# Kernel optimization log

Hardware: AMD Instinct MI355X
Metric: run time of the kernel (lower is better)

Reference implementation:

```python
import jax, jax.numpy as jnp
import numpy as np

KE = 14.3996454784255
P = 6  # polynomial cutoff order
A_EXP = 0.3
A_PREFACTOR = 0.4543
C = jnp.array([0.1818, 0.5099, 0.2802, 0.02817], dtype=jnp.float32)
K = jnp.array([3.2, 0.9423, 0.4028, 0.2016], dtype=jnp.float32)

N_NODES = 100000
N_EDGES = 6400000
N_ELEM = 10
N_RADII = 119


def setup_inputs() -> dict:
    key = jax.random.key(0)
    k1, k2, k3, k4, k5 = jax.random.split(key, 5)
    # edge distances in a physically plausible range (avoid x ~ 0 -> 1/x blowup)
    x = jax.random.uniform(k1, (N_EDGES, 1), dtype=jnp.float32) * 4.0 + 0.05
    node_attrs = jax.random.uniform(k2, (N_NODES, N_ELEM), dtype=jnp.float32)
    edge_index = jax.random.randint(k3, (2, N_EDGES), 0, N_NODES, dtype=jnp.int64)
    atomic_numbers = jax.random.randint(k4, (N_ELEM,), 1, N_RADII, dtype=jnp.int64)
    # covalent radii table (stand-in for ase.data.covalent_radii), ~0.3..2.6 Angstrom
    covalent_radii = 0.3 + 2.3 * jax.random.uniform(k5, (N_RADII,), dtype=jnp.float32)
    return {
        "x": x,
        "node_attrs": node_attrs,
        "edge_index": edge_index,
        "atomic_numbers": atomic_numbers,
        "covalent_radii": covalent_radii,
    }


def _envelope(x, r_max, p):
    r = x / r_max
    env = (1.0
           - (p + 1.0) * (p + 2.0) / 2.0 * r ** p
           + p * (p + 2.0) * r ** (p + 1)
           - p * (p + 1.0) / 2.0 * r ** (p + 2))
    return env * (x < r_max)


def reference(x, node_attrs, edge_index, atomic_numbers, covalent_radii):
    sender = edge_index[0]    # [E]
    receiver = edge_index[1]  # [E]
    # per-node atomic number from one-hot-ish node_attrs
    node_Z = atomic_numbers[jnp.argmax(node_attrs, axis=1)][:, None]  # [N,1] int
    Z_u = node_Z[sender]   # [E,1] int
    Z_v = node_Z[receiver] # [E,1] int
    Zu_f = Z_u.astype(x.dtype)
    Zv_f = Z_v.astype(x.dtype)
    a = A_PREFACTOR * 0.529 / (Zu_f ** A_EXP + Zv_f ** A_EXP)  # [E,1]
    r_over_a = x / a
    phi = (C[0] * jnp.exp(-K[0] * r_over_a)
           + C[1] * jnp.exp(-K[1] * r_over_a)
           + C[2] * jnp.exp(-K[2] * r_over_a)
           + C[3] * jnp.exp(-K[3] * r_over_a))
    v_edges = KE * Zu_f * Zv_f / x * phi  # [E,1]
    r_max = covalent_radii[Z_u[:, 0]][:, None] + covalent_radii[Z_v[:, 0]][:, None]  # [E,1]
    env = _envelope(x, r_max, float(P))
    v_edges = 0.5 * v_edges * env
    V_ZBL = jax.ops.segment_sum(v_edges, receiver, num_segments=node_attrs.shape[0])  # [N,1]
    return V_ZBL[:, 0]
```

## Files before the change

kernel.cpp:

```cpp
#include <hip/hip_runtime.h>

#define KE_CONST 14.3996454784255f

#define P2_SHIFT 15
#define P2_CHUNK 32768
#define MAXC     4
#define MAXE     16
#define ELEM_CAP 131072
#define DN_THR   1024
#define DN_BLOCKS 256
#define SCAN_THR 1024
#define SCAN_B   256
#define CNT_B    256
#define EB       32

__device__ __forceinline__ void scan_alloc(const unsigned* __restrict__ g_,
        int& nb0, int& nb1, int& nb2, int& nb3,
        int& st1, int& st2, int& st3,
        long long& g0, long long& g1, long long& g2, long long& g3) {
    g0 = g_[0]; g1 = g_[1]; g2 = g_[2]; g3 = g_[3];
    long long tot = g0 + g1 + g2 + g3; if (tot < 1) tot = 1;
    nb0 = (int)((g0 * SCAN_B) / tot); if (nb0 < 1) nb0 = 1;
    nb1 = (int)((g1 * SCAN_B) / tot); if (nb1 < 1) nb1 = 1;
    nb2 = (int)((g2 * SCAN_B) / tot); if (nb2 < 1) nb2 = 1;
    nb3 = (int)((g3 * SCAN_B) / tot); if (nb3 < 1) nb3 = 1;
    int sum = nb0 + nb1 + nb2 + nb3;
    while (sum > SCAN_B) {
        if      (nb0 >= nb1 && nb0 >= nb2 && nb0 >= nb3) nb0--;
        else if (nb1 >= nb2 && nb1 >= nb3)               nb1--;
        else if (nb2 >= nb3)                             nb2--;
        else                                             nb3--;
        sum--;
    }
    while (sum < SCAN_B) {
        if      (nb0 >= nb1 && nb0 >= nb2 && nb0 >= nb3) nb0++;
        else if (nb1 >= nb2 && nb1 >= nb3)               nb1++;
        else if (nb2 >= nb3)                             nb2++;
        else                                             nb3++;
        sum++;
    }
    st1 = nb0; st2 = nb0 + nb1; st3 = nb0 + nb1 + nb2;
}

__device__ __forceinline__ unsigned enc_val16(float xv, const float4& p) {
    float t = xv * p.x;
    float phi = 0.1818f  * __expf(-3.2f    * t)
              + 0.5099f  * __expf(-0.9423f * t)
              + 0.2802f  * __expf(-0.4028f * t)
              + 0.02817f * __expf(-0.2016f * t);
    float rr = xv * p.w;
    float r2 = rr * rr;
    float r6 = r2 * r2 * r2;
    float env = 1.0f - 28.0f * r6 + 48.0f * r6 * rr - 21.0f * r6 * r2;
    float val = fmaxf(p.y * phi / xv * env, 0.0f);
    unsigned e = (__float_as_uint(val) + 0x8000u) >> 16;
    return (xv < p.z) ? e : 0u;
}

__device__ __forceinline__ void scatter_bal(unsigned rw, float xv, const float4& p,
                                            unsigned* cur, const unsigned* seg,
                                            unsigned* __restrict__ packedB, int lane) {
    unsigned cc = rw >> P2_SHIFT;
    unsigned w  = ((rw & (P2_CHUNK - 1)) << 16) | enc_val16(xv, p);
    unsigned long long m0 = __ballot(cc == 0), m1 = __ballot(cc == 1),
                       m2 = __ballot(cc == 2), m3 = __ballot(cc == 3);
    unsigned long long mine = (cc == 0) ? m0 : (cc == 1) ? m1 : (cc == 2) ? m2 : m3;
    int ldr = __ffsll((long long)mine) - 1;
    unsigned base = 0;
    if (lane == ldr) base = atomicAdd(&cur[cc], (unsigned)__popcll(mine));
    base = __shfl(base, ldr, 64);
    unsigned pos = base + (unsigned)__popcll(mine & ((1ull << lane) - 1ull));
    packedB[(size_t)seg[cc] + pos] = w;
}

#define ACC1(W) { if ((W) & 0xFFFFu) \
    atomicAdd(&acc[(W) >> 16], __uint_as_float(((W) & 0xFFFFu) << 16)); }
#define ACC4(Q) { ACC1((Q).x); ACC1((Q).y); ACC1((Q).z); ACC1((Q).w); }

#define PREFIX_HIST(sb, h_lds, t)                                              \
    {                                                                          \
        const int c_ = (t) >> 8, bb_ = (t) & 255;                              \
        (sb)[t] = (h_lds)[bb_ * MAXC + c_];                                    \
        __syncthreads();                                                       \
        for (int off_ = 1; off_ < DN_BLOCKS; off_ <<= 1) {                     \
            unsigned add_ = (bb_ >= off_) ? (sb)[c_ * DN_BLOCKS + bb_ - off_]  \
                                          : 0u;                                \
            __syncthreads();                                                   \
            (sb)[t] += add_;                                                   \
            __syncthreads();                                                   \
        }                                                                      \
    }

__global__ __launch_bounds__(1024)
void zbl_prep(const float* __restrict__ node_attrs,
              const int* __restrict__ ei,
              const int* __restrict__ atomic_numbers,
              const float* __restrict__ covalent_radii,
              unsigned char* __restrict__ elem_g,
              float4* __restrict__ pair_tab,
              unsigned* __restrict__ hist,
              int n_edges, int n_elem, int n_nodes) {
    const int b = blockIdx.x, t = threadIdx.x, lane = t & 63;

    if (b < CNT_B) {
        __shared__ unsigned h[MAXC];
        if (t < MAXC) h[t] = 0u;
        __syncthreads();
        long long e0 = (((long long)b * n_edges) / CNT_B) & ~3LL;
        long long e1 = (b == CNT_B - 1) ? (long long)n_edges
                     : ((((long long)(b + 1) * n_edges) / CNT_B) & ~3LL);
        const int* r = ei + n_edges;
        unsigned c0 = 0, c1 = 0, c2 = 0, c3 = 0;
        long long vend = e1 & ~3LL;
        for (long long p = e0 + (long long)t * 4; p + 4 <= vend; p += 1024LL * 4) {
            int4 a = *(const int4*)(r + p);
            unsigned cc;
            cc = ((unsigned)a.x) >> P2_SHIFT; c0 += (cc==0); c1 += (cc==1); c2 += (cc==2); c3 += (cc==3);
            cc = ((unsigned)a.y) >> P2_SHIFT; c0 += (cc==0); c1 += (cc==1); c2 += (cc==2); c3 += (cc==3);
            cc = ((unsigned)a.z) >> P2_SHIFT; c0 += (cc==0); c1 += (cc==1); c2 += (cc==2); c3 += (cc==3);
            cc = ((unsigned)a.w) >> P2_SHIFT; c0 += (cc==0); c1 += (cc==1); c2 += (cc==2); c3 += (cc==3);
        }
        for (long long e2 = vend + t; e2 < e1; e2 += 1024) {
            unsigned cc = ((unsigned)r[e2]) >> P2_SHIFT;
            c0 += (cc==0); c1 += (cc==1); c2 += (cc==2); c3 += (cc==3);
        }
        for (int o = 32; o; o >>= 1) {
            c0 += __shfl_down(c0, o, 64); c1 += __shfl_down(c1, o, 64);
            c2 += __shfl_down(c2, o, 64); c3 += __shfl_down(c3, o, 64);
        }
        if (lane == 0) {
            atomicAdd(&h[0], c0); atomicAdd(&h[1], c1);
            atomicAdd(&h[2], c2); atomicAdd(&h[3], c3);
        }
        __syncthreads();
        if (t < MAXC) hist[b * MAXC + t] = h[t];
    } else if (b < CNT_B + EB) {
        int bb = b - CNT_B;
        int n0 = (int)(((long long)bb * n_nodes) / EB);
        int n1 = (int)(((long long)(bb + 1) * n_nodes) / EB);
        for (int n = n0 + t; n < n1; n += 1024) {
            const float* row = node_attrs + (size_t)n * n_elem;
            float best = row[0]; int bi = 0;
            for (int i = 1; i < n_elem; ++i) {
                float v = row[i];
                if (v > best) { best = v; bi = i; }
            }
            elem_g[n] = (unsigned char)bi;
        }
    } else {
        int np = n_elem * n_elem;
        if (t < np) {
            int eu = t / n_elem, ev = t - eu * n_elem;
            int Zu = atomic_numbers[eu], Zv = atomic_numbers[ev];
            float zu = (float)Zu, zv = (float)Zv;
            float inv_a = (__powf(zu, 0.3f) + __powf(zv, 0.3f)) * (1.0f / (0.4543f * 0.529f));
            float rmax  = covalent_radii[Zu] + covalent_radii[Zv];
            pair_tab[t] = make_float4(inv_a, 0.5f * KE_CONST * zu * zv, rmax, 1.0f / rmax);
        }
    }
}

__global__ __launch_bounds__(DN_THR)
void zbl_dense(const float* __restrict__ x,
               const int* __restrict__ ei,
               const unsigned char* __restrict__ elem_g,
               const float4* __restrict__ pair_tab,
               const unsigned* __restrict__ hist,
               unsigned* __restrict__ packedB,
               int n_edges, int n_elem, int n_nodes) {
    __shared__ __align__(16) unsigned char elem[ELEM_CAP];
    __shared__ float4 pt[MAXE * MAXE];
    __shared__ unsigned h_lds[DN_BLOCKS * MAXC];
    __shared__ unsigned sb[MAXC * DN_BLOCKS];
    __shared__ unsigned cur[MAXC], seg[MAXC];

    const int b = blockIdx.x, t = threadIdx.x, lane = t & 63;

    for (int i = t; i < DN_BLOCKS * MAXC; i += DN_THR) h_lds[i] = hist[i];
    __syncthreads();
    PREFIX_HIST(sb, h_lds, t);

    if (t == 0) {
        unsigned tot0 = sb[0 * DN_BLOCKS + 255];
        unsigned tot1 = sb[1 * DN_BLOCKS + 255];
        unsigned tot2 = sb[2 * DN_BLOCKS + 255];
        seg[0] = sb[0 * DN_BLOCKS + b] - h_lds[b * MAXC + 0];
        seg[1] = tot0 + sb[1 * DN_BLOCKS + b] - h_lds[b * MAXC + 1];
        seg[2] = tot0 + tot1 + sb[2 * DN_BLOCKS + b] - h_lds[b * MAXC + 2];
        seg[3] = tot0 + tot1 + tot2 + sb[3 * DN_BLOCKS + b] - h_lds[b * MAXC + 3];
        cur[0] = 0; cur[1] = 0; cur[2] = 0; cur[3] = 0;
    }

    int np = n_elem * n_elem;
    for (int i = t; i < np; i += DN_THR) pt[i] = pair_tab[i];
    {
        int nwords = (n_nodes + 15) >> 4;
        const uint4* eg4 = (const uint4*)elem_g;
        uint4* el4 = (uint4*)elem;
        for (int i = t; i < nwords; i += DN_THR) el4[i] = eg4[i];
    }
    __syncthreads();

    long long e0 = (((long long)b * n_edges) / DN_BLOCKS) & ~3LL;
    long long e1 = (b == DN_BLOCKS - 1) ? (long long)n_edges
                 : ((((long long)(b + 1) * n_edges) / DN_BLOCKS) & ~3LL);
    long long vend = e1 & ~3LL;

    for (long long p = e0 + (long long)t * 4; p + 4 <= vend; p += (long long)DN_THR * 4) {
        int4   s4 = *(const int4*)(ei + p);
        int4   r4 = *(const int4*)(ei + n_edges + p);
        float4 x4 = *(const float4*)(x + p);
        float4 p0 = pt[elem[s4.x] * n_elem + elem[r4.x]];
        float4 p1 = pt[elem[s4.y] * n_elem + elem[r4.y]];
        float4 p2 = pt[elem[s4.z] * n_elem + elem[r4.z]];
        float4 p3 = pt[elem[s4.w] * n_elem + elem[r4.w]];
        scatter_bal((unsigned)r4.x, x4.x, p0, cur, seg, packedB, lane);
        scatter_bal((unsigned)r4.y, x4.y, p1, cur, seg, packedB, lane);
        scatter_bal((unsigned)r4.z, x4.z, p2, cur, seg, packedB, lane);
        scatter_bal((unsigned)r4.w, x4.w, p3, cur, seg, packedB, lane);
    }
    for (long long e2 = vend + t; e2 < e1; e2 += DN_THR) {
        int rr = ei[n_edges + e2];
        float4 pp = pt[elem[ei[e2]] * n_elem + elem[rr]];
        scatter_bal((unsigned)rr, x[e2], pp, cur, seg, packedB, lane);
    }
}

__global__ __launch_bounds__(SCAN_THR)
void zbl_scan_c(const unsigned* __restrict__ packedB,
                const unsigned* __restrict__ hist,
                float* __restrict__ partial,
                unsigned* __restrict__ tot_ws) {
    __shared__ __align__(16) float acc[P2_CHUNK];
    __shared__ unsigned h_lds[DN_BLOCKS * MAXC];
    __shared__ unsigned sb[MAXC * DN_BLOCKS];
    __shared__ unsigned tot[MAXC];
    const int b = blockIdx.x, t = threadIdx.x;

    for (int i = t; i < DN_BLOCKS * MAXC; i += SCAN_THR) h_lds[i] = hist[i];
    for (int i = t * 4; i < P2_CHUNK; i += SCAN_THR * 4)
        *(float4*)&acc[i] = make_float4(0.f, 0.f, 0.f, 0.f);
    __syncthreads();
    PREFIX_HIST(sb, h_lds, t);
    {
        const int c_ = t >> 8, bb_ = t & 255;
        if (bb_ == 255) tot[c_] = sb[t];
    }
    __syncthreads();
    if (b == 0 && t < MAXC) tot_ws[t] = tot[t];

    int nb0, nb1, nb2, nb3, st1, st2, st3;
    long long g0, g1, g2, g3;
    scan_alloc(tot, nb0, nb1, nb2, nb3, st1, st2, st3, g0, g1, g2, g3);

    const int c   = (b >= st1) + (b >= st2) + (b >= st3);
    const int jb  = b - ((c == 0) ? 0 : (c == 1) ? st1 : (c == 2) ? st2 : st3);
    long long Tc  = (c == 0) ? g0 : (c == 1) ? g1 : (c == 2) ? g2 : g3;
    int nbc       = (c == 0) ? nb0 : (c == 1) ? nb1 : (c == 2) ? nb2 : nb3;
    long long csc = (c == 0) ? 0LL : (c == 1) ? g0 : (c == 2) ? g0 + g1 : g0 + g1 + g2;
    long long s = csc + Tc * jb / nbc;
    long long e = csc + Tc * (jb + 1) / nbc;

    if (s < e) {
        long long va = (s + 3) & ~3LL; if (va > e) va = e;
        long long ve = e & ~3LL;       if (ve < va) ve = va;
        for (long long i2 = s + t; i2 < va; i2 += SCAN_THR) {
            unsigned wd = packedB[i2]; ACC1(wd);
        }
        long long m  = ve - va;
        long long sq = (m >> 4) << 2;
        const unsigned* p0 = packedB + va;
        for (long long o = (long long)t * 4; o < sq; o += (long long)SCAN_THR * 4) {
            uint4 qa = *(const uint4*)(p0 + o);
            uint4 qb = *(const uint4*)(p0 + sq + o);
            uint4 qc = *(const uint4*)(p0 + 2 * sq + o);
            uint4 qd = *(const uint4*)(p0 + 3 * sq + o);
            ACC4(qa); ACC4(qb); ACC4(qc); ACC4(qd);
        }
        for (long long i2 = va + 4 * sq + (long long)t * 4; i2 + 4 <= ve;
             i2 += (long long)SCAN_THR * 4) {
            uint4 q = *(const uint4*)(packedB + i2);
            ACC4(q);
        }
        for (long long i2 = ve + t; i2 < e; i2 += SCAN_THR) {
            unsigned wd = packedB[i2]; ACC1(wd);
        }
    }

    __syncthreads();
    float* pp = partial + (size_t)b * P2_CHUNK;
    for (int i = t * 4; i < P2_CHUNK; i += SCAN_THR * 4)
        *(float4*)(pp + i) = *(const float4*)&acc[i];
}

__global__ void zbl_reduce_p(const float* __restrict__ partial,
                             const unsigned* __restrict__ tot_ws,
                             float* __restrict__ out,
                             int n_nodes) {
    int i = blockIdx.x * blockDim.x + threadIdx.x;
    if (i >= n_nodes) return;

    unsigned tt[MAXC] = { tot_ws[0], tot_ws[1], tot_ws[2], tot_ws[3] };
    int nb0, nb1, nb2, nb3, st1, st2, st3;
    long long g0, g1, g2, g3;
    scan_alloc(tt, nb0, nb1, nb2, nb3, st1, st2, st3, g0, g1, g2, g3);

    int c  = i >> P2_SHIFT;
    int li = i & (P2_CHUNK - 1);
    int st  = (c == 0) ? 0 : (c == 1) ? st1 : (c == 2) ? st2 : st3;
    int nbc = (c == 0) ? nb0 : (c == 1) ? nb1 : (c == 2) ? nb2 : nb3;
    const float* p = partial + (size_t)st * P2_CHUNK + li;
    float s0 = 0.f, s1 = 0.f, s2 = 0.f, s3 = 0.f;
    int j = 0;
    for (; j + 4 <= nbc; j += 4) {
        s0 += p[(size_t)(j + 0) * P2_CHUNK];
        s1 += p[(size_t)(j + 1) * P2_CHUNK];
        s2 += p[(size_t)(j + 2) * P2_CHUNK];
        s3 += p[(size_t)(j + 3) * P2_CHUNK];
    }
    for (; j < nbc; ++j) s0 += p[(size_t)j * P2_CHUNK];
    out[i] = (s0 + s1) + (s2 + s3);
}

__global__ void zbl_node_prep(const float* __restrict__ node_attrs,
                              const int* __restrict__ atomic_numbers,
                              const float* __restrict__ covalent_radii,
                              float4* __restrict__ node_data,
                              float* __restrict__ out_zero,
                              int n_nodes, int n_elem) {
    int n = blockIdx.x * blockDim.x + threadIdx.x;
    if (n >= n_nodes) return;
    const float* row = node_attrs + (size_t)n * n_elem;
    float best = row[0];
    int bi = 0;
    for (int i = 1; i < n_elem; ++i) {
        float v = row[i];
        if (v > best) { best = v; bi = i; }
    }
    int Z = atomic_numbers[bi];
    float zf = (float)Z;
    node_data[n] = make_float4(zf, __powf(zf, 0.3f), covalent_radii[Z], 0.0f);
    out_zero[n] = 0.0f;
}

__global__ void zbl_edge_atomic(const float* __restrict__ x,
                                const int* __restrict__ edge_index,
                                const float4* __restrict__ node_data,
                                float* __restrict__ out,
                                int n_edges) {
    int e = blockIdx.x * blockDim.x + threadIdx.x;
    if (e >= n_edges) return;
    int snd = edge_index[e];
    int r = edge_index[n_edges + e];
    float xv = x[e];
    float4 du = node_data[snd];
    float4 dv = node_data[r];
    float rmax = du.z + dv.z;
    if (xv >= rmax) return;
    const float inv_a_pref = 1.0f / (0.4543f * 0.529f);
    float t = xv * (du.y + dv.y) * inv_a_pref;
    float phi = 0.1818f  * __expf(-3.2f    * t)
              + 0.5099f  * __expf(-0.9423f * t)
              + 0.2802f  * __expf(-0.4028f * t)
              + 0.02817f * __expf(-0.2016f * t);
    float v = KE_CONST * du.x * dv.x * phi / xv;
    float rr = xv / rmax;
    float r2 = rr * rr;
    float r6 = r2 * r2 * r2;
    float env = 1.0f - 28.0f * r6 + 48.0f * r6 * rr - 21.0f * r6 * r2;
    atomicAdd(&out[r], 0.5f * v * env);
}

extern "C" void kernel_launch(void* const* d_in, const int* in_sizes, int n_in,
                              void* d_out, int out_size, void* d_ws, size_t ws_size,
                              hipStream_t stream) {
    const float* x              = (const float*)d_in[0];
    const float* node_attrs     = (const float*)d_in[1];
    const int*   edge_index     = (const int*)d_in[2];
    const int*   atomic_numbers = (const int*)d_in[3];
    const float* covalent_radii = (const float*)d_in[4];
    float* out = (float*)d_out;

    int n_edges = in_sizes[0];
    int n_elem  = in_sizes[3];
    int n_nodes = in_sizes[1] / n_elem;

    int C = (n_nodes + P2_CHUNK - 1) >> P2_SHIFT;
    size_t elem_bytes   = (((size_t)n_nodes) + 255) & ~(size_t)255;
    size_t pair_bytes   = ((size_t)MAXE * MAXE * sizeof(float4) + 255) & ~(size_t)255;
    size_t hist_bytes   = (((size_t)DN_BLOCKS * MAXC * 4 + 64) + 255) & ~(size_t)255;
    size_t packed_bytes = (((size_t)n_edges * sizeof(unsigned)) + 255) & ~(size_t)255;
    size_t part_bytes   = (size_t)SCAN_B * P2_CHUNK * sizeof(float);
    bool fast = (C >= 1) && (C <= MAXC) && (n_nodes <= ELEM_CAP) &&
                (n_elem >= 1) && (n_elem <= MAXE) &&
                (ws_size >= elem_bytes + pair_bytes + hist_bytes + packed_bytes + part_bytes);

    if (fast) {
        unsigned char* elem     = (unsigned char*)d_ws;
        float4*        pair_tab = (float4*)((char*)d_ws + elem_bytes);
        unsigned*      hist     = (unsigned*)((char*)d_ws + elem_bytes + pair_bytes);
        unsigned*      tot_ws   = hist + DN_BLOCKS * MAXC;
        unsigned*      packedB  = (unsigned*)((char*)d_ws + elem_bytes + pair_bytes + hist_bytes);
        float*         part     = (float*)((char*)d_ws + elem_bytes + pair_bytes + hist_bytes + packed_bytes);

        zbl_prep<<<CNT_B + EB + 1, 1024, 0, stream>>>(
            node_attrs, edge_index, atomic_numbers, covalent_radii,
            elem, pair_tab, hist, n_edges, n_elem, n_nodes);

        zbl_dense<<<DN_BLOCKS, DN_THR, 0, stream>>>(
            x, edge_index, elem, pair_tab, hist, packedB,
            n_edges, n_elem, n_nodes);

        zbl_scan_c<<<SCAN_B, SCAN_THR, 0, stream>>>(
            packedB, hist, part, tot_ws);

        zbl_reduce_p<<<(n_nodes + 255) / 256, 256, 0, stream>>>(
            part, tot_ws, out, n_nodes);
        return;
    }

    float4* node_data = (float4*)d_ws;
    zbl_node_prep<<<(n_nodes + 255) / 256, 256, 0, stream>>>(
        node_attrs, atomic_numbers, covalent_radii, node_data,
        out, n_nodes, n_elem);
    zbl_edge_atomic<<<(n_edges + 255) / 256, 256, 0, stream>>>(
        x, edge_index, node_data, out, n_edges);
}
```

Measured before the change: 176.8 us.

## Replace partial-buffer reduction kernel with direct atomic adds from LDS accumulators

Each scan block now flushes its 32K-entry LDS accumulator straight into the output with float atomicAdd, skipping zero entries. This removes the separate partial-sum reduce kernel and the large partial buffer it reads and writes (256 × 32K floats). Output zeroing moves into the prep kernel. Starting offsets are staggered per block to spread atomic contention, at the cost of many global atomics and a floating-point sum order that is no longer deterministic.

```diff
diff --git a/kernel.cpp b/kernel.cpp
--- a/kernel.cpp
+++ b/kernel.cpp
@@ -99,6 +99,7 @@
               unsigned char* __restrict__ elem_g,
               float4* __restrict__ pair_tab,
               unsigned* __restrict__ hist,
+              float* __restrict__ out,
               int n_edges, int n_elem, int n_nodes) {
     const int b = blockIdx.x, t = threadIdx.x, lane = t & 63;
 
@@ -146,6 +147,7 @@
                 if (v > best) { best = v; bi = i; }
             }
             elem_g[n] = (unsigned char)bi;
+            out[n] = 0.0f;
         }
     } else {
         int np = n_elem * n_elem;
@@ -227,10 +229,10 @@
 }
 
 __global__ __launch_bounds__(SCAN_THR)
-void zbl_scan_c(const unsigned* __restrict__ packedB,
+void zbl_scan_a(const unsigned* __restrict__ packedB,
                 const unsigned* __restrict__ hist,
-                float* __restrict__ partial,
-                unsigned* __restrict__ tot_ws) {
+                float* __restrict__ out,
+                int n_nodes) {
     __shared__ __align__(16) float acc[P2_CHUNK];
     __shared__ unsigned h_lds[DN_BLOCKS * MAXC];
     __shared__ unsigned sb[MAXC * DN_BLOCKS];
@@ -247,7 +249,6 @@
         if (bb_ == 255) tot[c_] = sb[t];
     }
     __syncthreads();
-    if (b == 0 && t < MAXC) tot_ws[t] = tot[t];
 
     int nb0, nb1, nb2, nb3, st1, st2, st3;
     long long g0, g1, g2, g3;
@@ -288,38 +289,26 @@
     }
 
     __syncthreads();
-    float* pp = partial + (size_t)b * P2_CHUNK;
-    for (int i = t * 4; i < P2_CHUNK; i += SCAN_THR * 4)
-        *(float4*)(pp + i) = *(const float4*)&acc[i];
-}
-
-__global__ void zbl_reduce_p(const float* __restrict__ partial,
-                             const unsigned* __restrict__ tot_ws,
-                             float* __restrict__ out,
-                             int n_nodes) {
-    int i = blockIdx.x * blockDim.x + threadIdx.x;
-    if (i >= n_nodes) return;
-
-    unsigned tt[MAXC] = { tot_ws[0], tot_ws[1], tot_ws[2], tot_ws[3] };
-    int nb0, nb1, nb2, nb3, st1, st2, st3;
-    long long g0, g1, g2, g3;
-    scan_alloc(tt, nb0, nb1, nb2, nb3, st1, st2, st3, g0, g1, g2, g3);
-
-    int c  = i >> P2_SHIFT;
-    int li = i & (P2_CHUNK - 1);
-    int st  = (c == 0) ? 0 : (c == 1) ? st1 : (c == 2) ? st2 : st3;
-    int nbc = (c == 0) ? nb0 : (c == 1) ? nb1 : (c == 2) ? nb2 : nb3;
-    const float* p = partial + (size_t)st * P2_CHUNK + li;
-    float s0 = 0.f, s1 = 0.f, s2 = 0.f, s3 = 0.f;
-    int j = 0;
-    for (; j + 4 <= nbc; j += 4) {
-        s0 += p[(size_t)(j + 0) * P2_CHUNK];
-        s1 += p[(size_t)(j + 1) * P2_CHUNK];
-        s2 += p[(size_t)(j + 2) * P2_CHUNK];
-        s3 += p[(size_t)(j + 3) * P2_CHUNK];
-    }
-    for (; j < nbc; ++j) s0 += p[(size_t)j * P2_CHUNK];
-    out[i] = (s0 + s1) + (s2 + s3);
+    {
+        long long nodebase = (long long)c << P2_SHIFT;
+        int start = (b * 388) & (P2_CHUNK - 1) & ~3;
+        for (int k = 0; k < P2_CHUNK; k += SCAN_THR * 4) {
+            int i = (start + k + t * 4) & (P2_CHUNK - 1);
+            float4 v = *(const float4*)&acc[i];
+            long long n4 = nodebase + i;
+            if (n4 + 3 < n_nodes) {
+                if (v.x != 0.f) atomicAdd(&out[n4 + 0], v.x);
+                if (v.y != 0.f) atomicAdd(&out[n4 + 1], v.y);
+                if (v.z != 0.f) atomicAdd(&out[n4 + 2], v.z);
+                if (v.w != 0.f) atomicAdd(&out[n4 + 3], v.w);
+            } else {
+                if (v.x != 0.f && n4 + 0 < n_nodes) atomicAdd(&out[n4 + 0], v.x);
+                if (v.y != 0.f && n4 + 1 < n_nodes) atomicAdd(&out[n4 + 1], v.y);
+                if (v.z != 0.f && n4 + 2 < n_nodes) atomicAdd(&out[n4 + 2], v.z);
+                if (v.w != 0.f && n4 + 3 < n_nodes) atomicAdd(&out[n4 + 3], v.w);
+            }
+        }
+    }
 }
 
 __global__ void zbl_node_prep(const float* __restrict__ node_attrs,
@@ -390,32 +379,26 @@
     size_t pair_bytes   = ((size_t)MAXE * MAXE * sizeof(float4) + 255) & ~(size_t)255;
     size_t hist_bytes   = (((size_t)DN_BLOCKS * MAXC * 4 + 64) + 255) & ~(size_t)255;
     size_t packed_bytes = (((size_t)n_edges * sizeof(unsigned)) + 255) & ~(size_t)255;
-    size_t part_bytes   = (size_t)SCAN_B * P2_CHUNK * sizeof(float);
     bool fast = (C >= 1) && (C <= MAXC) && (n_nodes <= ELEM_CAP) &&
                 (n_elem >= 1) && (n_elem <= MAXE) &&
-                (ws_size >= elem_bytes + pair_bytes + hist_bytes + packed_bytes + part_bytes);
+                (ws_size >= elem_bytes + pair_bytes + hist_bytes + packed_bytes);
 
     if (fast) {
         unsigned char* elem     = (unsigned char*)d_ws;
         float4*        pair_tab = (float4*)((char*)d_ws + elem_bytes);
         unsigned*      hist     = (unsigned*)((char*)d_ws + elem_bytes + pair_bytes);
-        unsigned*      tot_ws   = hist + DN_BLOCKS * MAXC;
         unsigned*      packedB  = (unsigned*)((char*)d_ws + elem_bytes + pair_bytes + hist_bytes);
-        float*         part     = (float*)((char*)d_ws + elem_bytes + pair_bytes + hist_bytes + packed_bytes);
 
         zbl_prep<<<CNT_B + EB + 1, 1024, 0, stream>>>(
             node_attrs, edge_index, atomic_numbers, covalent_radii,
-            elem, pair_tab, hist, n_edges, n_elem, n_nodes);
+            elem, pair_tab, hist, out, n_edges, n_elem, n_nodes);
 
         zbl_dense<<<DN_BLOCKS, DN_THR, 0, stream>>>(
             x, edge_index, elem, pair_tab, hist, packedB,
             n_edges, n_elem, n_nodes);
 
-        zbl_scan_c<<<SCAN_B, SCAN_THR, 0, stream>>>(
-            packedB, hist, part, tot_ws);
-
-        zbl_reduce_p<<<(n_nodes + 255) / 256, 256, 0, stream>>>(
-            part, tot_ws, out, n_nodes);
+        zbl_scan_a<<<SCAN_B, SCAN_THR, 0, stream>>>(
+            packedB, hist, out, n_nodes);
         return;
     }
 
```

New measurement: 248.7 us. 40.7% more time.

## Pack node element ids as 4-bit nibbles and simplify scan totals

Applied to the files above, without the earlier changes.

Element indices are packed two per byte, which halves the per-block LDS copy of the node→element table in the dense scatter kernel. This reduces the LDS footprint and the global-to-LDS staging traffic, which may allow better occupancy. The scan kernel no longer runs the full 256-block prefix over the histogram just to get per-chunk totals. It now sums the hist with wave shuffles and LDS atomics. The cost is extra shift/mask work on each element lookup.

```diff
diff --git a/kernel.cpp b/kernel.cpp
--- a/kernel.cpp
+++ b/kernel.cpp
@@ -6,7 +6,7 @@
 #define P2_CHUNK 32768
 #define MAXC     4
 #define MAXE     16
-#define ELEM_CAP 131072
+#define ELEM4_CAP 65536
 #define DN_THR   1024
 #define DN_BLOCKS 256
 #define SCAN_THR 1024
@@ -96,7 +96,7 @@
               const int* __restrict__ ei,
               const int* __restrict__ atomic_numbers,
               const float* __restrict__ covalent_radii,
-              unsigned char* __restrict__ elem_g,
+              unsigned char* __restrict__ elem4_g,
               float4* __restrict__ pair_tab,
               unsigned* __restrict__ hist,
               int n_edges, int n_elem, int n_nodes) {
@@ -136,16 +136,28 @@
         if (t < MAXC) hist[b * MAXC + t] = h[t];
     } else if (b < CNT_B + EB) {
         int bb = b - CNT_B;
-        int n0 = (int)(((long long)bb * n_nodes) / EB);
-        int n1 = (int)(((long long)(bb + 1) * n_nodes) / EB);
-        for (int n = n0 + t; n < n1; n += 1024) {
-            const float* row = node_attrs + (size_t)n * n_elem;
+        int npairs = (n_nodes + 1) >> 1;
+        int p0 = (int)(((long long)bb * npairs) / EB);
+        int p1 = (int)(((long long)(bb + 1) * npairs) / EB);
+        for (int p = p0 + t; p < p1; p += 1024) {
+            int n0 = 2 * p, n1 = 2 * p + 1;
+            const float* row = node_attrs + (size_t)n0 * n_elem;
             float best = row[0]; int bi = 0;
             for (int i = 1; i < n_elem; ++i) {
                 float v = row[i];
                 if (v > best) { best = v; bi = i; }
             }
-            elem_g[n] = (unsigned char)bi;
+            unsigned byte = (unsigned)bi;
+            if (n1 < n_nodes) {
+                const float* row2 = node_attrs + (size_t)n1 * n_elem;
+                float b2 = row2[0]; int bj = 0;
+                for (int i = 1; i < n_elem; ++i) {
+                    float v = row2[i];
+                    if (v > b2) { b2 = v; bj = i; }
+                }
+                byte |= ((unsigned)bj) << 4;
+            }
+            elem4_g[p] = (unsigned char)byte;
         }
     } else {
         int np = n_elem * n_elem;
@@ -163,12 +175,12 @@
 __global__ __launch_bounds__(DN_THR)
 void zbl_dense(const float* __restrict__ x,
                const int* __restrict__ ei,
-               const unsigned char* __restrict__ elem_g,
+               const unsigned char* __restrict__ elem4_g,
                const float4* __restrict__ pair_tab,
                const unsigned* __restrict__ hist,
                unsigned* __restrict__ packedB,
                int n_edges, int n_elem, int n_nodes) {
-    __shared__ __align__(16) unsigned char elem[ELEM_CAP];
+    __shared__ __align__(16) unsigned char elem4[ELEM4_CAP];
     __shared__ float4 pt[MAXE * MAXE];
     __shared__ unsigned h_lds[DN_BLOCKS * MAXC];
     __shared__ unsigned sb[MAXC * DN_BLOCKS];
@@ -194,9 +206,10 @@
     int np = n_elem * n_elem;
     for (int i = t; i < np; i += DN_THR) pt[i] = pair_tab[i];
     {
-        int nwords = (n_nodes + 15) >> 4;
-        const uint4* eg4 = (const uint4*)elem_g;
-        uint4* el4 = (uint4*)elem;
+        int nbytes = (n_nodes + 1) >> 1;
+        int nwords = (nbytes + 15) >> 4;
+        const uint4* eg4 = (const uint4*)elem4_g;
+        uint4* el4 = (uint4*)elem4;
         for (int i = t; i < nwords; i += DN_THR) el4[i] = eg4[i];
     }
     __syncthreads();
@@ -206,14 +219,16 @@
                  : ((((long long)(b + 1) * n_edges) / DN_BLOCKS) & ~3LL);
     long long vend = e1 & ~3LL;
 
+    #define EG(n) ((unsigned)((elem4[(unsigned)(n) >> 1] >> (((unsigned)(n) & 1u) << 2)) & 15u))
+
     for (long long p = e0 + (long long)t * 4; p + 4 <= vend; p += (long long)DN_THR * 4) {
         int4   s4 = *(const int4*)(ei + p);
         int4   r4 = *(const int4*)(ei + n_edges + p);
         float4 x4 = *(const float4*)(x + p);
-        float4 p0 = pt[elem[s4.x] * n_elem + elem[r4.x]];
-        float4 p1 = pt[elem[s4.y] * n_elem + elem[r4.y]];
-        float4 p2 = pt[elem[s4.z] * n_elem + elem[r4.z]];
-        float4 p3 = pt[elem[s4.w] * n_elem + elem[r4.w]];
+        float4 p0 = pt[EG(s4.x) * n_elem + EG(r4.x)];
+        float4 p1 = pt[EG(s4.y) * n_elem + EG(r4.y)];
+        float4 p2 = pt[EG(s4.z) * n_elem + EG(r4.z)];
+        float4 p3 = pt[EG(s4.w) * n_elem + EG(r4.w)];
         scatter_bal((unsigned)r4.x, x4.x, p0, cur, seg, packedB, lane);
         scatter_bal((unsigned)r4.y, x4.y, p1, cur, seg, packedB, lane);
         scatter_bal((unsigned)r4.z, x4.z, p2, cur, seg, packedB, lane);
@@ -221,30 +236,34 @@
     }
     for (long long e2 = vend + t; e2 < e1; e2 += DN_THR) {
         int rr = ei[n_edges + e2];
-        float4 pp = pt[elem[ei[e2]] * n_elem + elem[rr]];
+        float4 pp = pt[EG(ei[e2]) * n_elem + EG(rr)];
         scatter_bal((unsigned)rr, x[e2], pp, cur, seg, packedB, lane);
     }
+    #undef EG
 }
 
 __global__ __launch_bounds__(SCAN_THR)
-void zbl_scan_c(const unsigned* __restrict__ packedB,
+void zbl_scan_t(const unsigned* __restrict__ packedB,
                 const unsigned* __restrict__ hist,
                 float* __restrict__ partial,
                 unsigned* __restrict__ tot_ws) {
     __shared__ __align__(16) float acc[P2_CHUNK];
-    __shared__ unsigned h_lds[DN_BLOCKS * MAXC];
-    __shared__ unsigned sb[MAXC * DN_BLOCKS];
     __shared__ unsigned tot[MAXC];
     const int b = blockIdx.x, t = threadIdx.x;
 
-    for (int i = t; i < DN_BLOCKS * MAXC; i += SCAN_THR) h_lds[i] = hist[i];
+    if (t < MAXC) tot[t] = 0u;
     for (int i = t * 4; i < P2_CHUNK; i += SCAN_THR * 4)
         *(float4*)&acc[i] = make_float4(0.f, 0.f, 0.f, 0.f);
     __syncthreads();
-    PREFIX_HIST(sb, h_lds, t);
+
     {
-        const int c_ = t >> 8, bb_ = t & 255;
-        if (bb_ == 255) tot[c_] = sb[t];
+        unsigned v = hist[t];
+        int lane = t & 63;
+        v += __shfl_xor(v, 4, 64);
+        v += __shfl_xor(v, 8, 64);
+        v += __shfl_xor(v, 16, 64);
+        v += __shfl_xor(v, 32, 64);
+        if (lane < MAXC) atomicAdd(&tot[lane], v);
     }
     __syncthreads();
     if (b == 0 && t < MAXC) tot_ws[t] = tot[t];
@@ -386,17 +405,17 @@
     int n_nodes = in_sizes[1] / n_elem;
 
     int C = (n_nodes + P2_CHUNK - 1) >> P2_SHIFT;
-    size_t elem_bytes   = (((size_t)n_nodes) + 255) & ~(size_t)255;
+    size_t elem_bytes   = ((((size_t)n_nodes + 1) >> 1) + 255) & ~(size_t)255;
     size_t pair_bytes   = ((size_t)MAXE * MAXE * sizeof(float4) + 255) & ~(size_t)255;
     size_t hist_bytes   = (((size_t)DN_BLOCKS * MAXC * 4 + 64) + 255) & ~(size_t)255;
     size_t packed_bytes = (((size_t)n_edges * sizeof(unsigned)) + 255) & ~(size_t)255;
     size_t part_bytes   = (size_t)SCAN_B * P2_CHUNK * sizeof(float);
-    bool fast = (C >= 1) && (C <= MAXC) && (n_nodes <= ELEM_CAP) &&
+    bool fast = (C >= 1) && (C <= MAXC) && (n_nodes <= 2 * ELEM4_CAP) &&
                 (n_elem >= 1) && (n_elem <= MAXE) &&
                 (ws_size >= elem_bytes + pair_bytes + hist_bytes + packed_bytes + part_bytes);
 
     if (fast) {
-        unsigned char* elem     = (unsigned char*)d_ws;
+        unsigned char* elem4    = (unsigned char*)d_ws;
         float4*        pair_tab = (float4*)((char*)d_ws + elem_bytes);
         unsigned*      hist     = (unsigned*)((char*)d_ws + elem_bytes + pair_bytes);
         unsigned*      tot_ws   = hist + DN_BLOCKS * MAXC;
@@ -405,13 +424,13 @@
 
         zbl_prep<<<CNT_B + EB + 1, 1024, 0, stream>>>(
             node_attrs, edge_index, atomic_numbers, covalent_radii,
-            elem, pair_tab, hist, n_edges, n_elem, n_nodes);
+            elem4, pair_tab, hist, n_edges, n_elem, n_nodes);
 
         zbl_dense<<<DN_BLOCKS, DN_THR, 0, stream>>>(
-            x, edge_index, elem, pair_tab, hist, packedB,
+            x, edge_index, elem4, pair_tab, hist, packedB,
             n_edges, n_elem, n_nodes);
 
-        zbl_scan_c<<<SCAN_B, SCAN_THR, 0, stream>>>(
+        zbl_scan_t<<<SCAN_B, SCAN_THR, 0, stream>>>(
             packedB, hist, part, tot_ws);
 
         zbl_reduce_p<<<(n_nodes + 255) / 256, 256, 0, stream>>>(
```

After: 175.8 us. About the same (-0.6%).
